# Performance work log

Measured on AMD Instinct MI355X. Metric: run time of the kernel, lower is better.

The kernel has to match this reference:

```python
import jax, jax.numpy as jnp
import numpy as np

B, H0, W0, C, NH, A, P = 32, 56, 56, 256, 8, 49, 7  # P = pool_size = sqrt(agent_num)
KS = 3  # depthwise conv kernel


def setup_inputs() -> dict:
    key = jax.random.key(0)
    ks = jax.random.split(key, 12)
    f32 = jnp.float32
    inp = {
        "x": jax.random.normal(ks[0], (B, H0 * W0, C), f32),
        "qkv_w": jax.random.normal(ks[1], (C, 3 * C), f32) * 0.02,   # used as x @ qkv_w
        "qkv_b": jax.random.normal(ks[2], (3 * C,), f32) * 0.02,
        "proj_w": jax.random.normal(ks[3], (C, C), f32) * 0.02,
        "proj_b": jax.random.normal(ks[4], (C,), f32) * 0.02,
        "dwc_w": jax.random.normal(ks[5], (C, 1, KS, KS), f32) * 0.1,  # depthwise OIHW, groups=C
        "dwc_b": jnp.zeros((C,), f32),
        "an_bias": jax.random.normal(ks[6], (NH, A, 7, 7), f32) * 0.02,
        "na_bias": jax.random.normal(ks[7], (NH, A, 7, 7), f32) * 0.02,
        "ah_bias": jax.random.normal(ks[8], (1, NH, A, H0, 1), f32) * 0.02,
        "aw_bias": jax.random.normal(ks[9], (1, NH, A, 1, W0), f32) * 0.02,
        "ha_bias": jax.random.normal(ks[10], (1, NH, H0, 1, A), f32) * 0.02,
        "wa_bias": jax.random.normal(ks[11], (1, NH, 1, W0, A), f32) * 0.02,
        "h": H0,
        "w": W0,
    }
    return inp


def _resize(t, hw):
    # bilinear (half-pixel, align_corners=False) resize of the last two dims
    return jax.image.resize(t, t.shape[:-2] + tuple(hw), method="bilinear")


def reference(x, qkv_w, qkv_b, proj_w, proj_b, dwc_w, dwc_b,
              an_bias, na_bias, ah_bias, aw_bias, ha_bias, wa_bias, h, w):
    b, n, c = x.shape
    nh = an_bias.shape[0]
    hd = c // nh
    a = an_bias.shape[1]
    p = int(a ** 0.5)
    scale = hd ** -0.5

    qkv = x @ qkv_w + qkv_b                      # (b, n, 3c)
    q, k, v = jnp.split(qkv, 3, axis=-1)

    # agent tokens: adaptive avg pool of q over (h, w) -> (p, p); exact since h%p==0
    q_img = q.reshape(b, h, w, c)
    agent = q_img.reshape(b, p, h // p, p, w // p, c).mean(axis=(2, 4)).reshape(b, a, c)

    q = q.reshape(b, n, nh, hd).transpose(0, 2, 1, 3)       # (b, nh, n, hd)
    k = k.reshape(b, n, nh, hd).transpose(0, 2, 1, 3)
    v = v.reshape(b, n, nh, hd).transpose(0, 2, 1, 3)
    agent = agent.reshape(b, a, nh, hd).transpose(0, 2, 1, 3)  # (b, nh, a, hd)

    def agent2token_bias(bias):  # (nh, a, h0, w0) -> (1, nh, a, n)
        pb = _resize(bias, (h, w)).reshape(nh, p, p, h * w).transpose(0, 3, 1, 2)
        pb = _resize(pb, (p, p)).reshape(nh, h * w, a).transpose(0, 2, 1)
        return pb[None]

    def token2agent_bias(bias):  # (nh, a, h0, w0) -> (1, nh, n, a)
        ab = _resize(bias, (h, w)).reshape(nh, p, p, h * w).transpose(0, 3, 1, 2)
        ab = _resize(ab, (p, p)).reshape(nh, h * w, a)
        return ab[None]

    position_bias = agent2token_bias(an_bias) + agent2token_bias((ah_bias + aw_bias)[0])
    agent_bias = token2agent_bias(na_bias) + \
        token2agent_bias((ha_bias + wa_bias)[0].transpose(0, 3, 1, 2))

    # stage 1: agent tokens attend to keys/values
    agent_attn = jax.nn.softmax(
        jnp.einsum('bhad,bhnd->bhan', agent * scale, k) + position_bias, axis=-1)
    agent_v = jnp.einsum('bhan,bhnd->bhad', agent_attn, v)      # (b, nh, a, hd)

    # stage 2: queries attend to agent tokens
    q_attn = jax.nn.softmax(
        jnp.einsum('bhnd,bhad->bhna', q * scale, agent) + agent_bias, axis=-1)
    out = jnp.einsum('bhna,bhad->bhnd', q_attn, agent_v)        # (b, nh, n, hd)
    out = out.transpose(0, 2, 1, 3).reshape(b, n, c)

    # depthwise conv on v
    v_img = v.transpose(0, 2, 1, 3).reshape(b, h, w, c).transpose(0, 3, 1, 2)  # NCHW
    dwc = jax.lax.conv_general_dilated(
        v_img, dwc_w, window_strides=(1, 1), padding='SAME',
        feature_group_count=c, dimension_numbers=('NCHW', 'OIHW', 'NCHW'))
    dwc = dwc + dwc_b[None, :, None, None]
    out = out + dwc.transpose(0, 2, 3, 1).reshape(b, n, c)

    return out @ proj_w + proj_b
```

## Files before the change

### kernel.cpp

```cpp
#include <hip/hip_runtime.h>
#include <stdint.h>

#define B_ 32
#define H_ 56
#define W_ 56
#define N_ 3136
#define C_ 256
#define NH_ 8
#define HD_ 32
#define A_ 49
#define NCH_ 7
#define CHK_ 448
#define SCALE_ 0.17677669529663687f

typedef _Float16 h16;
typedef __attribute__((ext_vector_type(4))) _Float16 h16x4;
typedef __attribute__((ext_vector_type(8))) _Float16 h16x8;
typedef __attribute__((ext_vector_type(4))) float f32x4;

__device__ __forceinline__ void gload16(const void* g, void* l) {
  __builtin_amdgcn_global_load_lds(
      (const __attribute__((address_space(1))) unsigned int*)(uintptr_t)g,
      (__attribute__((address_space(3))) unsigned int*)(unsigned int)(uintptr_t)l,
      16, 0, 0);
}

__global__ __launch_bounds__(256)
void bias_kernel(const float* __restrict__ an, const float* __restrict__ na,
                 const float* __restrict__ ah, const float* __restrict__ aw,
                 const float* __restrict__ ha, const float* __restrict__ wa,
                 float* __restrict__ posb, float* __restrict__ agbt)
{
  const int hh = blockIdx.x / A_;
  const int ag = blockIdx.x % A_;
  __shared__ float an7[A_], na7[A_], ahv[H_], awv[W_], hav[H_], wav[W_];
  const int tid = threadIdx.x;
  if (tid < A_) {
    an7[tid] = an[(hh*A_ + ag)*A_ + tid];
    na7[tid] = na[(hh*A_ + ag)*A_ + tid];
  }
  if (tid < H_) {
    ahv[tid] = ah[(hh*A_ + ag)*H_ + tid];
    awv[tid] = aw[(hh*A_ + ag)*W_ + tid];
    hav[tid] = ha[(hh*H_ + tid)*A_ + ag];
    wav[tid] = wa[(hh*W_ + tid)*A_ + ag];
  }
  __syncthreads();
  for (int t = tid; t < N_; t += 256) {
    const int ty = t / W_, tx = t % W_;
    const float py = (ty + 0.5f)*0.125f - 0.5f;
    const float px = (tx + 0.5f)*0.125f - 0.5f;
    const int iy = (int)floorf(py), ix = (int)floorf(px);
    const float fy = py - (float)iy, fx = px - (float)ix;
    const int iy0 = min(max(iy, 0), 6), iy1 = min(iy + 1, 6);
    const int ix0 = min(max(ix, 0), 6), ix1 = min(ix + 1, 6);
    const float w00 = (1.f-fy)*(1.f-fx), w01 = (1.f-fy)*fx;
    const float w10 = fy*(1.f-fx),       w11 = fy*fx;
    const float ban = w00*an7[iy0*7+ix0] + w01*an7[iy0*7+ix1]
                    + w10*an7[iy1*7+ix0] + w11*an7[iy1*7+ix1];
    const float bna = w00*na7[iy0*7+ix0] + w01*na7[iy0*7+ix1]
                    + w10*na7[iy1*7+ix0] + w11*na7[iy1*7+ix1];
    posb[((size_t)(hh*A_ + ag))*N_ + t] = ban + ahv[ty] + awv[tx];
    agbt[((size_t)(hh*A_ + ag))*N_ + t] = bna + hav[ty] + wav[tx];
  }
}

__global__ __launch_bounds__(256)
void convx_kernel(const float* __restrict__ x, h16* __restrict__ xh)
{
  const size_t nchunk = (size_t)B_*N_*C_/8;
  const size_t stride = (size_t)gridDim.x * 256;
  for (size_t i = blockIdx.x*256 + threadIdx.x; i < nchunk; i += stride) {
    const float4 u = ((const float4*)x)[i*2];
    const float4 v = ((const float4*)x)[i*2+1];
    h16x8 o;
    o[0]=(h16)u.x; o[1]=(h16)u.y; o[2]=(h16)u.z; o[3]=(h16)u.w;
    o[4]=(h16)v.x; o[5]=(h16)v.y; o[6]=(h16)v.z; o[7]=(h16)v.w;
    ((h16x8*)xh)[i] = o;
  }
}

__global__ __launch_bounds__(256)
void convw_kernel(const float* __restrict__ qkvw, const float* __restrict__ projw,
                  const float* __restrict__ dwcw, const float* __restrict__ dwcb,
                  h16* __restrict__ wtq, h16* __restrict__ wtp, h16* __restrict__ w9t)
{
  const int bid = blockIdx.x, k = threadIdx.x;
  if (bid < 768) {
    wtq[bid*256 + k] = (h16)qkvw[(size_t)k*768 + bid];
  } else if (bid < 1024) {
    const int n = bid - 768;
    wtp[n*256 + k] = (h16)projw[(size_t)k*256 + n];
  } else {
    const int row = bid - 1024;
    w9t[row*256 + k] = (h16)(row < 9 ? dwcw[k*9 + row] : dwcb[k]);
  }
}

__device__ __forceinline__ void gemm_tile_128(
    const h16* __restrict__ Ag, const h16* __restrict__ Bg,
    int m0, int n0, char* lds, f32x4 acc[4][4], int lane, int wr, int wc, int tid)
{
  int aoff[4], boff[4];
  #pragma unroll
  for (int r = 0; r < 4; ++r) {
    const int row = wr*64 + r*16 + (lane & 15);
    const int ps  = (lane >> 4) ^ ((row >> 1) & 3);
    aoff[r] = row*64 + ps*16;
  }
  #pragma unroll
  for (int c = 0; c < 4; ++c) {
    const int nrow = wc*64 + c*16 + (lane & 15);
    const int ps   = (lane >> 4) ^ ((nrow >> 1) & 3);
    boff[c] = 8192 + nrow*64 + ps*16;
  }
  const int i0 = tid, i1 = tid + 256;
  const int r0 = i0 >> 2, s0 = (i0 & 3) ^ ((r0 >> 1) & 3);
  const int r1 = i1 >> 2, s1 = (i1 & 3) ^ ((r1 >> 1) & 3);

  auto stage = [&](int buf, int k0) {
    char* l = lds + buf*16384;
    gload16(Ag + (size_t)(m0 + r0)*256 + k0 + s0*8, l + i0*16);
    gload16(Ag + (size_t)(m0 + r1)*256 + k0 + s1*8, l + i1*16);
    gload16(Bg + (size_t)(n0 + r0)*256 + k0 + s0*8, l + 8192 + i0*16);
    gload16(Bg + (size_t)(n0 + r1)*256 + k0 + s1*8, l + 8192 + i1*16);
  };

  stage(0, 0);
  __syncthreads();
  int cur = 0;
  #pragma unroll
  for (int k0 = 0; k0 < 256; k0 += 32) {
    if (k0 + 32 < 256) stage(cur ^ 1, k0 + 32);
    char* l = lds + cur*16384;
    h16x8 af[4], bf[4];
    #pragma unroll
    for (int r = 0; r < 4; ++r) af[r] = *(const h16x8*)(l + aoff[r]);
    #pragma unroll
    for (int c = 0; c < 4; ++c) bf[c] = *(const h16x8*)(l + boff[c]);
    #pragma unroll
    for (int r = 0; r < 4; ++r)
      #pragma unroll
      for (int c = 0; c < 4; ++c)
        acc[r][c] = __builtin_amdgcn_mfma_f32_16x16x32_f16(af[r], bf[c], acc[r][c], 0, 0, 0);
    __syncthreads();
    cur ^= 1;
  }
}

__global__ __launch_bounds__(256)
void gemm_qkv_mfma(const h16* __restrict__ xh, const h16* __restrict__ wtq,
                   const float* __restrict__ qkvb,
                   h16* __restrict__ q, h16* __restrict__ k, h16* __restrict__ v)
{
  __shared__ __align__(16) char lds[32768];
  const int tid = threadIdx.x, lane = tid & 63, wid = tid >> 6;
  const int wr = wid & 1, wc = wid >> 1;
  const int bid = blockIdx.x;
  const int xcd = bid & 7, j = bid >> 3;
  const int mt = xcd + 8*(j/6), nt = j - 6*(j/6);
  const int m0 = mt*128, n0 = nt*128;
  f32x4 acc[4][4] = {};
  gemm_tile_128(xh, wtq, m0, n0, lds, acc, lane, wr, wc, tid);
  #pragma unroll
  for (int r = 0; r < 4; ++r) {
    #pragma unroll
    for (int reg = 0; reg < 4; ++reg) {
      const int m = m0 + wr*64 + r*16 + (lane >> 4)*4 + reg;
      const int bb = m / N_, t = m % N_;
      #pragma unroll
      for (int c = 0; c < 4; ++c) {
        const int n = n0 + wc*64 + c*16 + (lane & 15);
        const float val = acc[r][c][reg] + qkvb[n];
        const int part = n >> 8, cc = n & 255, hh = cc >> 5, d = cc & 31;
        h16* dst = (part == 0) ? q : ((part == 1) ? k : v);
        dst[(((size_t)(bb*NH_ + hh))*N_ + t)*HD_ + d] = (h16)val;
      }
    }
  }
}

__global__ __launch_bounds__(256)
void gemm_proj_mfma(const h16* __restrict__ preh, const h16* __restrict__ wtp,
                    const float* __restrict__ projb, float* __restrict__ out)
{
  __shared__ __align__(16) char lds[32768];
  const int tid = threadIdx.x, lane = tid & 63, wid = tid >> 6;
  const int wr = wid & 1, wc = wid >> 1;
  const int bid = blockIdx.x;
  const int xcd = bid & 7, j = bid >> 3;
  const int mt = xcd + 8*(j >> 1), nt = j & 1;
  const int m0 = mt*128, n0 = nt*128;
  f32x4 acc[4][4] = {};
  gemm_tile_128(preh, wtp, m0, n0, lds, acc, lane, wr, wc, tid);
  #pragma unroll
  for (int r = 0; r < 4; ++r) {
    #pragma unroll
    for (int reg = 0; reg < 4; ++reg) {
      const int m = m0 + wr*64 + r*16 + (lane >> 4)*4 + reg;
      #pragma unroll
      for (int c = 0; c < 4; ++c) {
        const int n = n0 + wc*64 + c*16 + (lane & 15);
        out[(size_t)m*256 + n] = acc[r][c][reg] + projb[n];
      }
    }
  }
}

__global__ __launch_bounds__(64)
void pool_kernel(const h16* __restrict__ q, float* __restrict__ agent)
{
  const int blk = blockIdx.x;
  const int ag = blk % A_;
  const int rem = blk / A_;
  const int tid = threadIdx.x;
  const int d = tid & 31, half = tid >> 5;
  const int ay = ag / 7, ax = ag % 7;
  const size_t base = (size_t)rem * N_ * HD_;
  float s = 0.f;
  #pragma unroll
  for (int it = 0; it < 32; ++it) {
    const int yy = half*4 + (it >> 3), xx = it & 7;
    const int t = (ay*8 + yy)*W_ + ax*8 + xx;
    s += (float)q[base + (size_t)t*HD_ + d];
  }
  s += __shfl_down(s, 32, 64);
  if (tid < 32) agent[(size_t)rem*A_*HD_ + ag*HD_ + d] = s * (1.f/64.f);
}

__global__ __launch_bounds__(256)
void stage1a_mfma(const h16* __restrict__ kmat, const h16* __restrict__ vmat,
                  const float* __restrict__ agent, const float* __restrict__ posb,
                  float* __restrict__ pm, float* __restrict__ pl, float* __restrict__ pacc)
{
  __shared__ __align__(16) h16 Kl[64*32];
  __shared__ __align__(16) h16 Vt[32*72];
  __shared__ __align__(16) h16 Sl[64*72];
  const int tid = threadIdx.x, lane = tid & 63, wid = tid >> 6;
  const int bx = blockIdx.x;
  const int ch = bx % NCH_;
  const int rem = bx / NCH_;
  const int hh = rem & 7;
  const size_t kvbase = (size_t)rem * N_ * HD_;
  const size_t agbase = (size_t)rem * A_ * HD_;
  const float* pb = posb + (size_t)hh*A_*N_;

  const int arow = wid*16 + (lane & 15);
  const int kc = (lane >> 4) * 8;
  h16x8 a_ag = {};
  if (arow < A_) {
    #pragma unroll
    for (int j = 0; j < 8; ++j)
      a_ag[j] = (h16)(agent[agbase + (size_t)arow*HD_ + kc + j] * SCALE_);
  }

  const int r_k = tid >> 2;
  const int s_k = (tid & 3) ^ ((r_k >> 1) & 3);
  const int rowm = (lane >> 4) * 4;
  const int agrow0 = wid*16 + rowm;

  float m_r[4], l_r[4];
  #pragma unroll
  for (int r = 0; r < 4; ++r) { m_r[r] = -1e30f; l_r[r] = 0.f; }
  f32x4 accv[2] = {};

  for (int it = 0; it < 7; ++it) {
    const int t0 = ch*CHK_ + it*64;
    __syncthreads();
    gload16(kmat + kvbase + (size_t)(t0 + r_k)*HD_ + s_k*8, ((char*)Kl) + tid*16);
    const h16x8 vv = *(const h16x8*)&vmat[kvbase + (size_t)(t0 + lane)*HD_ + wid*8];
    #pragma unroll
    for (int j = 0; j < 8; ++j) Vt[(wid*8 + j)*72 + lane] = vv[j];
    __syncthreads();

    float sv[4][4];
    #pragma unroll
    for (int c = 0; c < 4; ++c) {
      const int kr = c*16 + (lane & 15);
      const int ph = (lane >> 4) ^ ((kr >> 1) & 3);
      const h16x8 bf = *(const h16x8*)&Kl[kr*32 + ph*8];
      const f32x4 sc = __builtin_amdgcn_mfma_f32_16x16x32_f16(a_ag, bf, (f32x4){0.f,0.f,0.f,0.f}, 0, 0, 0);
      #pragma unroll
      for (int reg = 0; reg < 4; ++reg) sv[reg][c] = sc[reg];
    }
    #pragma unroll
    for (int reg = 0; reg < 4; ++reg) {
      const int ag = agrow0 + reg;
      if (ag < A_) {
        #pragma unroll
        for (int c = 0; c < 4; ++c)
          sv[reg][c] += pb[(size_t)ag*N_ + t0 + c*16 + (lane & 15)];
      } else {
        #pragma unroll
        for (int c = 0; c < 4; ++c) sv[reg][c] = -1e30f;
      }
      float rm = fmaxf(fmaxf(sv[reg][0], sv[reg][1]), fmaxf(sv[reg][2], sv[reg][3]));
      rm = fmaxf(rm, __shfl_xor(rm, 1));
      rm = fmaxf(rm, __shfl_xor(rm, 2));
      rm = fmaxf(rm, __shfl_xor(rm, 4));
      rm = fmaxf(rm, __shfl_xor(rm, 8));
      const float mn = fmaxf(m_r[reg], rm);
      const float f = __expf(m_r[reg] - mn);
      m_r[reg] = mn;
      float rs = 0.f;
      #pragma unroll
      for (int c = 0; c < 4; ++c) {
        const float p = __expf(sv[reg][c] - mn);
        sv[reg][c] = p;
        rs += p;
      }
      rs += __shfl_xor(rs, 1); rs += __shfl_xor(rs, 2);
      rs += __shfl_xor(rs, 4); rs += __shfl_xor(rs, 8);
      l_r[reg] = l_r[reg]*f + rs;
      accv[0][reg] *= f;
      accv[1][reg] *= f;
      const int row = agrow0 + reg;
      #pragma unroll
      for (int c = 0; c < 4; ++c)
        Sl[row*72 + c*16 + (lane & 15)] = (h16)sv[reg][c];
    }
    __syncthreads();
    const int srow = wid*16 + (lane & 15);
    #pragma unroll
    for (int ks = 0; ks < 2; ++ks) {
      const h16x8 pf = *(const h16x8*)&Sl[srow*72 + ks*32 + (lane >> 4)*8];
      #pragma unroll
      for (int c2 = 0; c2 < 2; ++c2) {
        const int d = c2*16 + (lane & 15);
        const h16x8 vf = *(const h16x8*)&Vt[d*72 + ks*32 + (lane >> 4)*8];
        accv[c2] = __builtin_amdgcn_mfma_f32_16x16x32_f16(pf, vf, accv[c2], 0, 0, 0);
      }
    }
  }

  #pragma unroll
  for (int reg = 0; reg < 4; ++reg) {
    const int ag = agrow0 + reg;
    if (ag < A_) {
      if ((lane & 15) == 0) {
        pm[bx*A_ + ag] = m_r[reg];
        pl[bx*A_ + ag] = l_r[reg];
      }
      #pragma unroll
      for (int c2 = 0; c2 < 2; ++c2)
        pacc[(size_t)bx*(A_*HD_) + (size_t)ag*HD_ + c2*16 + (lane & 15)] = accv[c2][reg];
    }
  }
}

__global__ __launch_bounds__(256)
void stage1b_kernel(const float* __restrict__ pm, const float* __restrict__ pl,
                    const float* __restrict__ pacc, float* __restrict__ agv)
{
  const int rem = blockIdx.x;
  __shared__ float fs[NCH_*A_];
  const int tid = threadIdx.x;
  if (tid < A_) {
    float m = -1e30f;
    #pragma unroll
    for (int ch = 0; ch < NCH_; ++ch) m = fmaxf(m, pm[(rem*NCH_+ch)*A_ + tid]);
    float e[NCH_], l = 0.f;
    #pragma unroll
    for (int ch = 0; ch < NCH_; ++ch) {
      e[ch] = __expf(pm[(rem*NCH_+ch)*A_ + tid] - m);
      l += e[ch] * pl[(rem*NCH_+ch)*A_ + tid];
    }
    const float inv = 1.f / l;
    #pragma unroll
    for (int ch = 0; ch < NCH_; ++ch) fs[ch*A_ + tid] = e[ch] * inv;
  }
  __syncthreads();
  for (int idx = tid; idx < A_*HD_; idx += 256) {
    const int ag = idx >> 5;
    float s = 0.f;
    #pragma unroll
    for (int ch = 0; ch < NCH_; ++ch)
      s += fs[ch*A_ + ag] * pacc[((size_t)(rem*NCH_+ch))*(A_*HD_) + idx];
    agv[(size_t)rem*(A_*HD_) + idx] = s;
  }
}

__global__ __launch_bounds__(256)
void stage2_mfma(const h16* __restrict__ qmat, const float* __restrict__ agent,
                 const float* __restrict__ agv, const float* __restrict__ agbt,
                 h16* __restrict__ preh)
{
  __shared__ __align__(16) char lds2[45568];
  h16* Asw = (h16*)lds2;
  h16* AVt = (h16*)(lds2 + 4096);
  const int tid = threadIdx.x, lane = tid & 63, wid = tid >> 6;
  const int b = blockIdx.y >> 3, hh = blockIdx.y & 7;
  const size_t agbase = (size_t)(b*NH_ + hh)*A_*HD_;

  for (int i = tid; i < 64*32; i += 256) Asw[i] = (h16)0.f;
  for (int i = tid; i < 32*72; i += 256) AVt[i] = (h16)0.f;
  __syncthreads();
  for (int i = tid; i < A_*HD_; i += 256) {
    const int a = i >> 5, d = i & 31;
    Asw[a*32 + (((d >> 3) ^ ((a >> 1) & 3)))*8 + (d & 7)] = (h16)(agent[agbase + i] * SCALE_);
    AVt[d*72 + a] = (h16)agv[agbase + i];
  }
  __syncthreads();

  const int t0 = blockIdx.x*256 + wid*64;
  if (t0 >= N_) return;

  h16* Pl = (h16*)(lds2 + 8704 + wid*9216);
  const h16* qbase = qmat + (size_t)(b*NH_ + hh)*N_*HD_;
  const float* agbt_h = agbt + (size_t)hh*A_*N_;
  const int l15 = lane & 15, g = lane >> 4;

  h16x8 bq[4];
  #pragma unroll
  for (int c = 0; c < 4; ++c) {
    const int a = c*16 + l15;
    const int ph = g ^ ((a >> 1) & 3);
    bq[c] = *(const h16x8*)&Asw[a*32 + ph*8];
  }
  h16x8 aq[4];
  #pragma unroll
  for (int rt = 0; rt < 4; ++rt)
    aq[rt] = *(const h16x8*)&qbase[(size_t)(t0 + rt*16 + l15)*HD_ + g*8];

  f32x4 sc[4][4];
  #pragma unroll
  for (int rt = 0; rt < 4; ++rt)
    #pragma unroll
    for (int c = 0; c < 4; ++c)
      sc[rt][c] = __builtin_amdgcn_mfma_f32_16x16x32_f16(aq[rt], bq[c], (f32x4){0.f,0.f,0.f,0.f}, 0, 0, 0);

  #pragma unroll
  for (int rt = 0; rt < 4; ++rt) {
    float sv[4][4];
    #pragma unroll
    for (int c = 0; c < 4; ++c) {
      const int a = c*16 + l15;
      if (a < A_) {
        const float4 bias = *(const float4*)&agbt_h[(size_t)a*N_ + t0 + rt*16 + g*4];
        sv[0][c] = sc[rt][c][0] + bias.x;
        sv[1][c] = sc[rt][c][1] + bias.y;
        sv[2][c] = sc[rt][c][2] + bias.z;
        sv[3][c] = sc[rt][c][3] + bias.w;
      } else {
        sv[0][c] = sv[1][c] = sv[2][c] = sv[3][c] = -1e30f;
      }
    }
    #pragma unroll
    for (int reg = 0; reg < 4; ++reg) {
      float rm = fmaxf(fmaxf(sv[reg][0], sv[reg][1]), fmaxf(sv[reg][2], sv[reg][3]));
      rm = fmaxf(rm, __shfl_xor(rm, 1));
      rm = fmaxf(rm, __shfl_xor(rm, 2));
      rm = fmaxf(rm, __shfl_xor(rm, 4));
      rm = fmaxf(rm, __shfl_xor(rm, 8));
      float rs = 0.f;
      #pragma unroll
      for (int c = 0; c < 4; ++c) {
        const float p = __expf(sv[reg][c] - rm);
        sv[reg][c] = p;
        rs += p;
      }
      rs += __shfl_xor(rs, 1); rs += __shfl_xor(rs, 2);
      rs += __shfl_xor(rs, 4); rs += __shfl_xor(rs, 8);
      const float inv = 1.f / rs;
      const int row = rt*16 + g*4 + reg;
      #pragma unroll
      for (int c = 0; c < 4; ++c)
        Pl[row*72 + c*16 + l15] = (h16)(sv[reg][c] * inv);
    }
  }

  h16x8 vf[2][2];
  #pragma unroll
  for (int ks = 0; ks < 2; ++ks)
    #pragma unroll
    for (int c2 = 0; c2 < 2; ++c2)
      vf[ks][c2] = *(const h16x8*)&AVt[(c2*16 + l15)*72 + ks*32 + g*8];

  f32x4 av[4][2] = {};
  #pragma unroll
  for (int rt = 0; rt < 4; ++rt) {
    #pragma unroll
    for (int ks = 0; ks < 2; ++ks) {
      const h16x8 pf = *(const h16x8*)&Pl[(rt*16 + l15)*72 + ks*32 + g*8];
      #pragma unroll
      for (int c2 = 0; c2 < 2; ++c2)
        av[rt][c2] = __builtin_amdgcn_mfma_f32_16x16x32_f16(pf, vf[ks][c2], av[rt][c2], 0, 0, 0);
    }
  }

  #pragma unroll
  for (int rt = 0; rt < 4; ++rt)
    #pragma unroll
    for (int c2 = 0; c2 < 2; ++c2)
      #pragma unroll
      for (int reg = 0; reg < 4; ++reg) {
        const int t = t0 + rt*16 + g*4 + reg;
        preh[((size_t)b*N_ + t)*C_ + hh*HD_ + c2*16 + l15] = (h16)av[rt][c2][reg];
      }
}

__global__ __launch_bounds__(256)
void dwc_kernel(const h16* __restrict__ v, const h16* __restrict__ w9t,
                h16* __restrict__ preh)
{
  const int lin = blockIdx.x*256 + threadIdx.x;
  const int rem = blockIdx.y;
  const int t = lin >> 2, c8 = lin & 3;
  const int y = t / W_, x = t - y*W_;
  const int hh = rem & 7, b = rem >> 3;
  const int cbase = hh*HD_ + c8*8;

  h16x8 wk[9];
  #pragma unroll
  for (int k = 0; k < 9; ++k)
    wk[k] = *(const h16x8*)&w9t[k*C_ + cbase];
  h16x8 acc = *(const h16x8*)&w9t[9*C_ + cbase];

  const h16* vb = v + (size_t)rem*N_*HD_ + c8*8;
  #pragma unroll
  for (int ky = 0; ky < 3; ++ky) {
    #pragma unroll
    for (int kx = 0; kx < 3; ++kx) {
      const int yy = y + ky - 1, xx = x + kx - 1;
      const bool ok = ((unsigned)yy < (unsigned)H_) && ((unsigned)xx < (unsigned)W_);
      const int tt = ok ? (yy*W_ + xx) : t;
      const h16x8 vv = *(const h16x8*)&vb[(size_t)tt*HD_];
      const h16x8 w = ok ? wk[ky*3+kx] : (h16x8)(h16)0.f;
      acc += vv * w;
    }
  }

  h16x8* ph = (h16x8*)&preh[((size_t)b*N_ + t)*C_ + cbase];
  *ph += acc;
}

extern "C" void kernel_launch(void* const* d_in, const int* in_sizes, int n_in,
                              void* d_out, int out_size, void* d_ws, size_t ws_size,
                              hipStream_t stream)
{
  (void)in_sizes; (void)n_in; (void)out_size;
  const float* x     = (const float*)d_in[0];
  const float* qkvw  = (const float*)d_in[1];
  const float* qkvb  = (const float*)d_in[2];
  const float* projw = (const float*)d_in[3];
  const float* projb = (const float*)d_in[4];
  const float* dwcw  = (const float*)d_in[5];
  const float* dwcb  = (const float*)d_in[6];
  const float* an    = (const float*)d_in[7];
  const float* na    = (const float*)d_in[8];
  const float* ah    = (const float*)d_in[9];
  const float* aw    = (const float*)d_in[10];
  const float* ha    = (const float*)d_in[11];
  const float* wa    = (const float*)d_in[12];

  const size_t EL = (size_t)B_*N_*C_;
  char* ws = (char*)d_ws;
  h16*   qh    = (h16*)(ws);
  h16*   kh    = (h16*)(ws + EL*2);
  h16*   vh    = (h16*)(ws + EL*4);
  h16*   xh    = (h16*)(ws + EL*6);
  float* posb  = (float*)(ws + EL*8);
  float* agbt  = (float*)(ws + EL*8 + (size_t)NH_*A_*N_*4);
  float* agent = (float*)(ws + EL*8 + (size_t)NH_*A_*N_*8);
  float* agv   = (float*)(ws + EL*8 + (size_t)NH_*A_*N_*8 + (size_t)B_*NH_*A_*HD_*4);
  h16*   wtq   = (h16*)(ws + EL*8 + (size_t)NH_*A_*N_*8 + (size_t)B_*NH_*A_*HD_*8);
  h16*   wtp   = (h16*)((char*)wtq + (size_t)768*256*2);
  h16*   w9t   = (h16*)((char*)wtp + (size_t)256*256*2);
  const size_t NEED = EL*8 + (size_t)NH_*A_*N_*8 + (size_t)B_*NH_*A_*HD_*8
                    + (size_t)768*256*2 + (size_t)256*256*2 + (size_t)10*256*2;
  if (ws_size < NEED) return;

  float* pm   = (float*)xh;
  float* pl   = pm + (size_t)B_*NH_*NCH_*A_;
  float* pacc = pl + (size_t)B_*NH_*NCH_*A_;
  h16*   preh = kh;

  bias_kernel<<<dim3(NH_*A_), dim3(256), 0, stream>>>(an, na, ah, aw, ha, wa, posb, agbt);
  convx_kernel<<<dim3(4096), dim3(256), 0, stream>>>(x, xh);
  convw_kernel<<<dim3(1034), dim3(256), 0, stream>>>(qkvw, projw, dwcw, dwcb, wtq, wtp, w9t);
  gemm_qkv_mfma<<<dim3(4704), dim3(256), 0, stream>>>(xh, wtq, qkvb, qh, kh, vh);
  pool_kernel<<<dim3(B_*NH_*A_), dim3(64), 0, stream>>>(qh, agent);
  stage1a_mfma<<<dim3(B_*NH_*NCH_), dim3(256), 0, stream>>>(kh, vh, agent, posb, pm, pl, pacc);
  stage1b_kernel<<<dim3(B_*NH_), dim3(256), 0, stream>>>(pm, pl, pacc, agv);
  stage2_mfma<<<dim3(13, B_*NH_), dim3(256), 0, stream>>>(qh, agent, agv, agbt, preh);
  dwc_kernel<<<dim3(N_*4/256, B_*NH_), dim3(256), 0, stream>>>(vh, w9t, preh);
  gemm_proj_mfma<<<dim3(1568), dim3(256), 0, stream>>>(preh, wtp, projb, (float*)d_out);
}
```

Before: 321.5 us.

## Fuse fp32-to-fp16 conversion of x into QKV GEMM with 256-row tiles

```diff
diff --git a/kernel.cpp b/kernel.cpp
--- a/kernel.cpp
+++ b/kernel.cpp
@@ -66,21 +66,6 @@
 }
 
 __global__ __launch_bounds__(256)
-void convx_kernel(const float* __restrict__ x, h16* __restrict__ xh)
-{
-  const size_t nchunk = (size_t)B_*N_*C_/8;
-  const size_t stride = (size_t)gridDim.x * 256;
-  for (size_t i = blockIdx.x*256 + threadIdx.x; i < nchunk; i += stride) {
-    const float4 u = ((const float4*)x)[i*2];
-    const float4 v = ((const float4*)x)[i*2+1];
-    h16x8 o;
-    o[0]=(h16)u.x; o[1]=(h16)u.y; o[2]=(h16)u.z; o[3]=(h16)u.w;
-    o[4]=(h16)v.x; o[5]=(h16)v.y; o[6]=(h16)v.z; o[7]=(h16)v.w;
-    ((h16x8*)xh)[i] = o;
-  }
-}
-
-__global__ __launch_bounds__(256)
 void convw_kernel(const float* __restrict__ qkvw, const float* __restrict__ projw,
                   const float* __restrict__ dwcw, const float* __restrict__ dwcb,
                   h16* __restrict__ wtq, h16* __restrict__ wtp, h16* __restrict__ w9t)
@@ -97,6 +82,113 @@
   }
 }
 
+__global__ __launch_bounds__(512)
+void gemm_qkv_mfma(const float* __restrict__ x, const h16* __restrict__ wtq,
+                   const float* __restrict__ qkvb,
+                   h16* __restrict__ q, h16* __restrict__ k, h16* __restrict__ v)
+{
+  __shared__ __align__(16) char lds[49152];
+  const int tid = threadIdx.x, lane = tid & 63, wid = tid >> 6;
+  const int wr = wid & 3, wc = wid >> 2;
+  const int l15 = lane & 15, g = lane >> 4;
+  const int bid = blockIdx.x;
+  const int xcd = bid & 7, j = bid >> 3;
+  const int mt = xcd + 8*(j/6), nt = j - 6*(j/6);
+  const int m0 = mt*256, n0 = nt*128;
+
+  int aoff[4], boff[4];
+  #pragma unroll
+  for (int r = 0; r < 4; ++r) {
+    const int row = wr*64 + r*16 + l15;
+    const int ps  = g ^ ((row >> 1) & 3);
+    aoff[r] = row*64 + ps*16;
+  }
+  #pragma unroll
+  for (int c = 0; c < 4; ++c) {
+    const int nrow = wc*64 + c*16 + l15;
+    const int ps   = g ^ ((nrow >> 1) & 3);
+    boff[c] = 16384 + nrow*64 + ps*16;
+  }
+
+  const int ra0 = tid >> 2,         sa0 = (tid & 3) ^ ((ra0 >> 1) & 3);
+  const int ra1 = (tid + 512) >> 2, sa1 = (tid & 3) ^ ((ra1 >> 1) & 3);
+  const int rb = tid >> 2,          sb = (tid & 3) ^ ((rb >> 1) & 3);
+
+  const float* ax0 = x + (size_t)(m0 + ra0)*256 + sa0*8;
+  const float* ax1 = x + (size_t)(m0 + ra1)*256 + sa1*8;
+  const h16*   bx  = wtq + (size_t)(n0 + rb)*256 + sb*8;
+
+  f32x4 acc[4][4] = {};
+
+  {
+    const float4 u0 = *(const float4*)(ax0 + 0), u1 = *(const float4*)(ax0 + 4);
+    const float4 u2 = *(const float4*)(ax1 + 0), u3 = *(const float4*)(ax1 + 4);
+    gload16(bx, lds + 16384 + tid*16);
+    h16x8 o0, o1;
+    o0[0]=(h16)u0.x; o0[1]=(h16)u0.y; o0[2]=(h16)u0.z; o0[3]=(h16)u0.w;
+    o0[4]=(h16)u1.x; o0[5]=(h16)u1.y; o0[6]=(h16)u1.z; o0[7]=(h16)u1.w;
+    o1[0]=(h16)u2.x; o1[1]=(h16)u2.y; o1[2]=(h16)u2.z; o1[3]=(h16)u2.w;
+    o1[4]=(h16)u3.x; o1[5]=(h16)u3.y; o1[6]=(h16)u3.z; o1[7]=(h16)u3.w;
+    *(h16x8*)(lds + tid*16)         = o0;
+    *(h16x8*)(lds + (tid+512)*16)   = o1;
+  }
+  __syncthreads();
+
+  int cur = 0;
+  #pragma unroll
+  for (int k0 = 0; k0 < 256; k0 += 32) {
+    const bool has_next = (k0 + 32) < 256;
+    float4 u0, u1, u2, u3;
+    if (has_next) {
+      u0 = *(const float4*)(ax0 + k0 + 32);
+      u1 = *(const float4*)(ax0 + k0 + 36);
+      u2 = *(const float4*)(ax1 + k0 + 32);
+      u3 = *(const float4*)(ax1 + k0 + 36);
+      gload16(bx + k0 + 32, lds + (cur^1)*24576 + 16384 + tid*16);
+    }
+    char* l = lds + cur*24576;
+    h16x8 af[4], bf[4];
+    #pragma unroll
+    for (int r = 0; r < 4; ++r) af[r] = *(const h16x8*)(l + aoff[r]);
+    #pragma unroll
+    for (int c = 0; c < 4; ++c) bf[c] = *(const h16x8*)(l + boff[c]);
+    #pragma unroll
+    for (int r = 0; r < 4; ++r)
+      #pragma unroll
+      for (int c = 0; c < 4; ++c)
+        acc[r][c] = __builtin_amdgcn_mfma_f32_16x16x32_f16(af[r], bf[c], acc[r][c], 0, 0, 0);
+    if (has_next) {
+      char* ln = lds + (cur^1)*24576;
+      h16x8 o0, o1;
+      o0[0]=(h16)u0.x; o0[1]=(h16)u0.y; o0[2]=(h16)u0.z; o0[3]=(h16)u0.w;
+      o0[4]=(h16)u1.x; o0[5]=(h16)u1.y; o0[6]=(h16)u1.z; o0[7]=(h16)u1.w;
+      o1[0]=(h16)u2.x; o1[1]=(h16)u2.y; o1[2]=(h16)u2.z; o1[3]=(h16)u2.w;
+      o1[4]=(h16)u3.x; o1[5]=(h16)u3.y; o1[6]=(h16)u3.z; o1[7]=(h16)u3.w;
+      *(h16x8*)(ln + tid*16)       = o0;
+      *(h16x8*)(ln + (tid+512)*16) = o1;
+    }
+    __syncthreads();
+    cur ^= 1;
+  }
+
+  #pragma unroll
+  for (int r = 0; r < 4; ++r) {
+    #pragma unroll
+    for (int reg = 0; reg < 4; ++reg) {
+      const int m = m0 + wr*64 + r*16 + g*4 + reg;
+      const int bb = m / N_, t = m % N_;
+      #pragma unroll
+      for (int c = 0; c < 4; ++c) {
+        const int n = n0 + wc*64 + c*16 + l15;
+        const float val = acc[r][c][reg] + qkvb[n];
+        const int part = n >> 8, cc = n & 255, hh = cc >> 5, d = cc & 31;
+        h16* dst = (part == 0) ? q : ((part == 1) ? k : v);
+        dst[(((size_t)(bb*NH_ + hh))*N_ + t)*HD_ + d] = (h16)val;
+      }
+    }
+  }
+}
+
 __device__ __forceinline__ void gemm_tile_128(
     const h16* __restrict__ Ag, const h16* __restrict__ Bg,
     int m0, int n0, char* lds, f32x4 acc[4][4], int lane, int wr, int wc, int tid)
@@ -145,38 +237,6 @@
         acc[r][c] = __builtin_amdgcn_mfma_f32_16x16x32_f16(af[r], bf[c], acc[r][c], 0, 0, 0);
     __syncthreads();
     cur ^= 1;
-  }
-}
-
-__global__ __launch_bounds__(256)
-void gemm_qkv_mfma(const h16* __restrict__ xh, const h16* __restrict__ wtq,
-                   const float* __restrict__ qkvb,
-                   h16* __restrict__ q, h16* __restrict__ k, h16* __restrict__ v)
-{
-  __shared__ __align__(16) char lds[32768];
-  const int tid = threadIdx.x, lane = tid & 63, wid = tid >> 6;
-  const int wr = wid & 1, wc = wid >> 1;
-  const int bid = blockIdx.x;
-  const int xcd = bid & 7, j = bid >> 3;
-  const int mt = xcd + 8*(j/6), nt = j - 6*(j/6);
-  const int m0 = mt*128, n0 = nt*128;
-  f32x4 acc[4][4] = {};
-  gemm_tile_128(xh, wtq, m0, n0, lds, acc, lane, wr, wc, tid);
-  #pragma unroll
-  for (int r = 0; r < 4; ++r) {
-    #pragma unroll
-    for (int reg = 0; reg < 4; ++reg) {
-      const int m = m0 + wr*64 + r*16 + (lane >> 4)*4 + reg;
-      const int bb = m / N_, t = m % N_;
-      #pragma unroll
-      for (int c = 0; c < 4; ++c) {
-        const int n = n0 + wc*64 + c*16 + (lane & 15);
-        const float val = acc[r][c][reg] + qkvb[n];
-        const int part = n >> 8, cc = n & 255, hh = cc >> 5, d = cc & 31;
-        h16* dst = (part == 0) ? q : ((part == 1) ? k : v);
-        dst[(((size_t)(bb*NH_ + hh))*N_ + t)*HD_ + d] = (h16)val;
-      }
-    }
   }
 }
 
@@ -558,7 +618,7 @@
   h16*   qh    = (h16*)(ws);
   h16*   kh    = (h16*)(ws + EL*2);
   h16*   vh    = (h16*)(ws + EL*4);
-  h16*   xh    = (h16*)(ws + EL*6);
+  char*  scratch = ws + EL*6;
   float* posb  = (float*)(ws + EL*8);
   float* agbt  = (float*)(ws + EL*8 + (size_t)NH_*A_*N_*4);
   float* agent = (float*)(ws + EL*8 + (size_t)NH_*A_*N_*8);
@@ -570,15 +630,14 @@
                     + (size_t)768*256*2 + (size_t)256*256*2 + (size_t)10*256*2;
   if (ws_size < NEED) return;
 
-  float* pm   = (float*)xh;
+  float* pm   = (float*)scratch;
   float* pl   = pm + (size_t)B_*NH_*NCH_*A_;
   float* pacc = pl + (size_t)B_*NH_*NCH_*A_;
   h16*   preh = kh;
 
   bias_kernel<<<dim3(NH_*A_), dim3(256), 0, stream>>>(an, na, ah, aw, ha, wa, posb, agbt);
-  convx_kernel<<<dim3(4096), dim3(256), 0, stream>>>(x, xh);
   convw_kernel<<<dim3(1034), dim3(256), 0, stream>>>(qkvw, projw, dwcw, dwcb, wtq, wtp, w9t);
-  gemm_qkv_mfma<<<dim3(4704), dim3(256), 0, stream>>>(xh, wtq, qkvb, qh, kh, vh);
+  gemm_qkv_mfma<<<dim3(2352), dim3(512), 0, stream>>>(x, wtq, qkvb, qh, kh, vh);
   pool_kernel<<<dim3(B_*NH_*A_), dim3(64), 0, stream>>>(qh, agent);
   stage1a_mfma<<<dim3(B_*NH_*NCH_), dim3(256), 0, stream>>>(kh, vh, agent, posb, pm, pl, pacc);
   stage1b_kernel<<<dim3(B_*NH_), dim3(256), 0, stream>>>(pm, pl, pacc, agv);
```

New measurement: 359.2 us. 1.12x slower.
